# Optimization experiments

Measured on AMD Instinct MI355X. Metric: run time of the kernel, lower is better.

The kernel has to match this reference:

```python
import jax, jax.numpy as jnp
import numpy as np

N_NODES = 100000
N_EDGES = 1600000
DIMS = [21, 32, 64, 128, 21]  # conv1..conv4 (conv4 in-dim fixed to 128; source's 100 is a bug)


def _glorot(key, fan_in, fan_out):
    s = jnp.sqrt(6.0 / (fan_in + fan_out))
    return jax.random.uniform(key, (fan_in, fan_out), jnp.float32, -s, s)


def setup_inputs() -> dict:
    key = jax.random.key(0)
    ks = jax.random.split(key, 6)
    x = jax.random.normal(ks[0], (N_NODES, DIMS[0]), jnp.float32)
    edge_index = jax.random.randint(ks[1], (2, N_EDGES), 0, N_NODES, jnp.int64)
    inp = {"x": x, "edge_index": edge_index}
    wkeys = jax.random.split(ks[2], 4)
    for i in range(4):
        inp[f"W{i+1}"] = _glorot(wkeys[i], DIMS[i], DIMS[i + 1])
        inp[f"b{i+1}"] = jnp.zeros((DIMS[i + 1],), jnp.float32)
    return inp


def gcn_conv(x, row, col, W, b):
    # PyG GCNConv: h = x W; symmetric normalization with self loops; aggregate; + bias
    N = x.shape[0]
    h = x @ W  # [N, F]
    deg = jnp.zeros((N,), h.dtype).at[col].add(1.0) + 1.0  # +1 for self loop
    dinv = jax.lax.rsqrt(deg)
    norm = dinv[row] * dinv[col]  # [E]
    agg = jnp.zeros_like(h).at[col].add(norm[:, None] * h[row])  # scatter messages
    agg = agg + (dinv * dinv)[:, None] * h  # self-loop contribution
    return agg + b


def reference(x, edge_index, W1, b1, W2, b2, W3, b3, W4, b4):
    row, col = edge_index[0], edge_index[1]
    x = jax.nn.relu(gcn_conv(x, row, col, W1, b1))
    x = jax.nn.relu(gcn_conv(x, row, col, W2, b2))
    x = jax.nn.relu(gcn_conv(x, row, col, W3, b3))
    x = gcn_conv(x, row, col, W4, b4)
    return x
```

## Files before the change

kernel.cpp:

```cpp
#include <hip/hip_runtime.h>
#include <hip/hip_fp16.h>

#define NN 100000
#define NE 1600000
#define SH 7
#define NB_BKT 782
#define BCAP 3072
#define CSRCAP 3200
#define CHUNK 8192
#define TILES_TOTAL 3125
#define PIPE_BLOCKS 512

static inline int cdiv(long long a, int b) { return (int)((a + b - 1) / b); }

__device__ inline float4 ld_h4(const float2* __restrict__ base, size_t idx) {
    float2 v = base[idx];
    const __half2* p = (const __half2*)&v;
    float2 f0 = __half22float2(p[0]);
    float2 f1 = __half22float2(p[1]);
    return make_float4(f0.x, f0.y, f1.x, f1.y);
}

__global__ void partition_kernel(const int* __restrict__ row, const int* __restrict__ col,
                                 int* __restrict__ bcur,
                                 unsigned int* __restrict__ packed, int E) {
    __shared__ int lh[NB_BKT];
    __shared__ int lbase[NB_BKT];
    for (int i = threadIdx.x; i < NB_BKT; i += 256) lh[i] = 0;
    __syncthreads();
    int base = blockIdx.x * CHUNK;
    int end = min(base + CHUNK, E);
    for (int e = base + threadIdx.x; e < end; e += 256) atomicAdd(&lh[col[e] >> SH], 1);
    __syncthreads();
    for (int i = threadIdx.x; i < NB_BKT; i += 256) {
        int v = lh[i];
        lbase[i] = v ? atomicAdd(&bcur[i], v) : 0;
        lh[i] = 0;
    }
    __syncthreads();
    for (int e = base + threadIdx.x; e < end; e += 256) {
        int c = col[e];
        int r = row[e];
        int b = c >> SH;
        int off = atomicAdd(&lh[b], 1);
        packed[lbase[b] + off] = ((unsigned)r << 7) | (unsigned)(c & 127);
    }
}

__global__ void bucket_nodes_place(const unsigned int* __restrict__ packed,
                                   const int* __restrict__ bcur, int* __restrict__ rowptr,
                                   int* __restrict__ rowend, float* __restrict__ dinv,
                                   int* __restrict__ csr_row, int N) {
    int b = blockIdx.x;
    __shared__ int lcnt[128];
    __shared__ int lcur[128];
    __shared__ int wt4[4];
    int t = threadIdx.x;
    if (t < 128) lcnt[t] = 0;
    __syncthreads();
    int s = b * BCAP;
    int e = bcur[b];
    for (int i = s + t; i < e; i += 256)
        atomicAdd(&lcnt[packed[i] & 127u], 1);
    __syncthreads();
    int node = (b << SH) + t;
    int v = (t < 128 && node < N) ? lcnt[t] + 1 : 0;
    int lane = t & 63, w = t >> 6;
    int incl = v;
#pragma unroll
    for (int off = 1; off < 64; off <<= 1) {
        int u = __shfl_up(incl, off, 64);
        if (lane >= off) incl += u;
    }
    if (lane == 63) wt4[w] = incl;
    __syncthreads();
    int woff = 0;
    for (int i = 0; i < w; i++) woff += wt4[i];
    int excl = woff + incl - v;
    if (t < 128 && node < N) {
        int start = b * CSRCAP + excl;
        rowptr[node] = start;
        rowend[node] = start + v;
        csr_row[start] = node;
        dinv[node] = rsqrtf((float)v);
        lcur[t] = start + 1;
    }
    __syncthreads();
    for (int i = s + t; i < e; i += 256) {
        unsigned p = packed[i];
        int r = (int)(p >> 7);
        int pos = atomicAdd(&lcur[p & 127u], 1);
        csr_row[pos] = r;
    }
}

__global__ void padx_kernel(const float* __restrict__ x, float* __restrict__ xp,
                            int* __restrict__ bcur, int N) {
    int idx = blockIdx.x * blockDim.x + threadIdx.x;
    if (idx < NB_BKT) bcur[idx] = idx * BCAP;
    if (idx >= N * 32) return;
    int n = idx >> 5;
    int k = idx & 31;
    xp[idx] = (k < 21) ? x[n * 21 + k] : 0.f;
}

template <int LPN, int FIN, int FOUT, int RJ, int OSTRIDE, bool HALF_OUT, bool HALF_IN>
__global__ __launch_bounds__(512) void gather_gemm(
    const float4* __restrict__ h, const int* __restrict__ rowptr,
    const int* __restrict__ rowend, const int* __restrict__ csr_row,
    const float* __restrict__ dinv, const float* __restrict__ W,
    const float* __restrict__ b, float* __restrict__ out, int N) {
    constexpr int NT = 512 / LPN;
    constexpr int FINP = 4 * LPN;
    constexpr int XLD = FINP + 1;
    constexpr int JG = FOUT / RJ;
    __shared__ float xs[NT * XLD];
    __shared__ float Ws[FIN * FOUT];
    __shared__ float bs[FOUT];
    const int t = threadIdx.x;
    const float2* hf2 = (const float2*)h;

    for (int i = t; i < FIN * FOUT; i += 512) Ws[i] = W[i];
    if (t < FOUT) bs[t] = b[t];

    const int l = t % LPN;
    const int ny = t / LPN;
    const int node = blockIdx.x * NT + ny;
    float4 acc = make_float4(0.f, 0.f, 0.f, 0.f);
    if (node < N) {
        int s = rowptr[node], e = rowend[node];
        float dn = dinv[node];
        int i = s;
        for (; i + 3 < e; i += 4) {
            int r0 = csr_row[i], r1 = csr_row[i + 1], r2 = csr_row[i + 2], r3 = csr_row[i + 3];
            float w0 = dinv[r0] * dn, w1 = dinv[r1] * dn, w2 = dinv[r2] * dn, w3 = dinv[r3] * dn;
            float4 a0, a1, a2, a3;
            if constexpr (HALF_IN) {
                a0 = ld_h4(hf2, (size_t)r0 * LPN + l);
                a1 = ld_h4(hf2, (size_t)r1 * LPN + l);
                a2 = ld_h4(hf2, (size_t)r2 * LPN + l);
                a3 = ld_h4(hf2, (size_t)r3 * LPN + l);
            } else {
                a0 = h[(size_t)r0 * LPN + l];
                a1 = h[(size_t)r1 * LPN + l];
                a2 = h[(size_t)r2 * LPN + l];
                a3 = h[(size_t)r3 * LPN + l];
            }
            acc.x = fmaf(w0, a0.x, acc.x); acc.y = fmaf(w0, a0.y, acc.y);
            acc.z = fmaf(w0, a0.z, acc.z); acc.w = fmaf(w0, a0.w, acc.w);
            acc.x = fmaf(w1, a1.x, acc.x); acc.y = fmaf(w1, a1.y, acc.y);
            acc.z = fmaf(w1, a1.z, acc.z); acc.w = fmaf(w1, a1.w, acc.w);
            acc.x = fmaf(w2, a2.x, acc.x); acc.y = fmaf(w2, a2.y, acc.y);
            acc.z = fmaf(w2, a2.z, acc.z); acc.w = fmaf(w2, a2.w, acc.w);
            acc.x = fmaf(w3, a3.x, acc.x); acc.y = fmaf(w3, a3.y, acc.y);
            acc.z = fmaf(w3, a3.z, acc.z); acc.w = fmaf(w3, a3.w, acc.w);
        }
        for (; i < e; i++) {
            int r0 = csr_row[i];
            float w0 = dinv[r0] * dn;
            float4 a0;
            if constexpr (HALF_IN) a0 = ld_h4(hf2, (size_t)r0 * LPN + l);
            else                   a0 = h[(size_t)r0 * LPN + l];
            acc.x = fmaf(w0, a0.x, acc.x); acc.y = fmaf(w0, a0.y, acc.y);
            acc.z = fmaf(w0, a0.z, acc.z); acc.w = fmaf(w0, a0.w, acc.w);
        }
    }
    xs[ny * XLD + 4 * l + 0] = acc.x;
    xs[ny * XLD + 4 * l + 1] = acc.y;
    xs[ny * XLD + 4 * l + 2] = acc.z;
    xs[ny * XLD + 4 * l + 3] = acc.w;
    __syncthreads();

    const int jg = t % JG;
    const int ng = t / JG;
    float r[RJ];
#pragma unroll
    for (int jj = 0; jj < RJ; jj++) r[jj] = 0.f;
#pragma unroll 4
    for (int k = 0; k < FIN; k++) {
        float xv = xs[ng * XLD + k];
#pragma unroll
        for (int jj = 0; jj < RJ; jj++)
            r[jj] = fmaf(xv, Ws[k * FOUT + jg * RJ + jj], r[jj]);
    }
    int onode = blockIdx.x * NT + ng;
    if (onode < N) {
#pragma unroll
        for (int jj = 0; jj < RJ; jj++) r[jj] = fmaxf(r[jj] + bs[jg * RJ + jj], 0.f);
        if constexpr (HALF_OUT) {
            if constexpr (RJ == 8) {
                float4 pk;
                __half2* ph = (__half2*)&pk;
                ph[0] = __float22half2_rn(make_float2(r[0], r[1]));
                ph[1] = __float22half2_rn(make_float2(r[2], r[3]));
                ph[2] = __float22half2_rn(make_float2(r[4], r[5]));
                ph[3] = __float22half2_rn(make_float2(r[6], r[7]));
                *(float4*)((__half*)out + (size_t)onode * FOUT + jg * RJ) = pk;
            } else {
                static_assert(!HALF_OUT || RJ == 8 || RJ == 4, "half path needs RJ 4 or 8");
                float2 pk;
                __half2* ph = (__half2*)&pk;
                ph[0] = __float22half2_rn(make_float2(r[0], r[1]));
                ph[1] = __float22half2_rn(make_float2(r[2], r[3]));
                *(float2*)((__half*)out + (size_t)onode * FOUT + jg * RJ) = pk;
            }
        } else {
            float* orow = out + (size_t)onode * OSTRIDE + jg * RJ;
#pragma unroll
            for (int c = 0; c < RJ / 4; c++)
                *(float4*)&orow[4 * c] = make_float4(r[4 * c], r[4 * c + 1], r[4 * c + 2], r[4 * c + 3]);
        }
    }
}

template <int LPN, bool BIAS, bool STORE21, bool HALF_IN>
__global__ void gather4_kernel(const float4* __restrict__ h, const int* __restrict__ rowptr,
                               const int* __restrict__ rowend, const int* __restrict__ csr_row,
                               const float* __restrict__ dinv, const float* __restrict__ bias,
                               float* __restrict__ outp, int N) {
    int node = blockIdx.x * blockDim.y + threadIdx.y;
    if (node >= N) return;
    int l = threadIdx.x;
    int s = rowptr[node], e = rowend[node];
    float dn = dinv[node];
    const float2* hf2 = (const float2*)h;
    float4 acc = make_float4(0.f, 0.f, 0.f, 0.f);
    int i = s;
    for (; i + 3 < e; i += 4) {
        int r0 = csr_row[i], r1 = csr_row[i + 1], r2 = csr_row[i + 2], r3 = csr_row[i + 3];
        float w0 = dinv[r0] * dn, w1 = dinv[r1] * dn, w2 = dinv[r2] * dn, w3 = dinv[r3] * dn;
        float4 a0, a1, a2, a3;
        if constexpr (HALF_IN) {
            a0 = ld_h4(hf2, (size_t)r0 * LPN + l);
            a1 = ld_h4(hf2, (size_t)r1 * LPN + l);
            a2 = ld_h4(hf2, (size_t)r2 * LPN + l);
            a3 = ld_h4(hf2, (size_t)r3 * LPN + l);
        } else {
            a0 = h[(size_t)r0 * LPN + l];
            a1 = h[(size_t)r1 * LPN + l];
            a2 = h[(size_t)r2 * LPN + l];
            a3 = h[(size_t)r3 * LPN + l];
        }
        acc.x = fmaf(w0, a0.x, acc.x); acc.y = fmaf(w0, a0.y, acc.y);
        acc.z = fmaf(w0, a0.z, acc.z); acc.w = fmaf(w0, a0.w, acc.w);
        acc.x = fmaf(w1, a1.x, acc.x); acc.y = fmaf(w1, a1.y, acc.y);
        acc.z = fmaf(w1, a1.z, acc.z); acc.w = fmaf(w1, a1.w, acc.w);
        acc.x = fmaf(w2, a2.x, acc.x); acc.y = fmaf(w2, a2.y, acc.y);
        acc.z = fmaf(w2, a2.z, acc.z); acc.w = fmaf(w2, a2.w, acc.w);
        acc.x = fmaf(w3, a3.x, acc.x); acc.y = fmaf(w3, a3.y, acc.y);
        acc.z = fmaf(w3, a3.z, acc.z); acc.w = fmaf(w3, a3.w, acc.w);
    }
    for (; i < e; i++) {
        int r0 = csr_row[i];
        float w0 = dinv[r0] * dn;
        float4 a0;
        if constexpr (HALF_IN) a0 = ld_h4(hf2, (size_t)r0 * LPN + l);
        else                   a0 = h[(size_t)r0 * LPN + l];
        acc.x = fmaf(w0, a0.x, acc.x); acc.y = fmaf(w0, a0.y, acc.y);
        acc.z = fmaf(w0, a0.z, acc.z); acc.w = fmaf(w0, a0.w, acc.w);
    }
    if (STORE21) {
        int j = 4 * l;
        float v[4] = {acc.x, acc.y, acc.z, acc.w};
#pragma unroll
        for (int c = 0; c < 4; c++) {
            int jj = j + c;
            if (jj < 21) outp[(size_t)node * 21 + jj] = v[c] + (BIAS ? bias[jj] : 0.f);
        }
    } else {
        ((float4*)outp)[(size_t)node * LPN + l] = acc;
    }
}

__device__ inline void fma_h8(const float4& v, float w, float4& a0, float4& a1) {
    const __half2* hh = (const __half2*)&v;
    float2 f0 = __half22float2(hh[0]);
    float2 f1 = __half22float2(hh[1]);
    float2 f2 = __half22float2(hh[2]);
    float2 f3 = __half22float2(hh[3]);
    a0.x = fmaf(w, f0.x, a0.x); a0.y = fmaf(w, f0.y, a0.y);
    a0.z = fmaf(w, f1.x, a0.z); a0.w = fmaf(w, f1.y, a0.w);
    a1.x = fmaf(w, f2.x, a1.x); a1.y = fmaf(w, f2.y, a1.y);
    a1.z = fmaf(w, f3.x, a1.z); a1.w = fmaf(w, f3.y, a1.w);
}

__global__ __launch_bounds__(512, 4) void gather_gemm_l3l4_pipe(
    const float4* __restrict__ h, const int* __restrict__ rowptr,
    const int* __restrict__ rowend, const int* __restrict__ csr_row,
    const float* __restrict__ dinv, const float* __restrict__ W3,
    const float* __restrict__ b3, const float* __restrict__ W4,
    float* __restrict__ out, int N) {
    __shared__ float xs[2][32 * 65];
    __shared__ float4 W3v[64 * 32];
    __shared__ float4 W4v[16 * 48];
    __shared__ float b3s[128];
    const int t = threadIdx.x;
    const int b = blockIdx.x;

    for (int sid = t; sid < 64 * 32; sid += 512) {
        int k = sid >> 5, q = sid & 31;
        int jg = q >> 2, c = q & 3;
        W3v[(k << 5) + (c << 3) + jg] = ((const float4*)W3)[sid];
    }
    for (int cid = t; cid < 16 * 48; cid += 512) {
        int i = cid / 48, rem = cid - i * 48;
        int jq = rem >> 3, jg = rem & 7;
        int k = jg * 16 + i;
        float v0 = (4 * jq + 0 < 21) ? W4[k * 21 + 4 * jq + 0] : 0.f;
        float v1 = (4 * jq + 1 < 21) ? W4[k * 21 + 4 * jq + 1] : 0.f;
        float v2 = (4 * jq + 2 < 21) ? W4[k * 21 + 4 * jq + 2] : 0.f;
        float v3 = (4 * jq + 3 < 21) ? W4[k * 21 + 4 * jq + 3] : 0.f;
        W4v[cid] = make_float4(v0, v1, v2, v3);
    }
    if (t < 128) b3s[t] = b3[t];
    __syncthreads();

    const int R = (TILES_TOTAL - b + PIPE_BLOCKS - 1) / PIPE_BLOCKS;

    for (int r = 0; r <= R; r++) {
        if (t < 256) {
            if (r < R) {
                const int l = t & 7;
                const int ny = t >> 3;
                const int node = (b + PIPE_BLOCKS * r) * 32 + ny;
                float4 acc0 = make_float4(0.f, 0.f, 0.f, 0.f);
                float4 acc1 = make_float4(0.f, 0.f, 0.f, 0.f);
                if (node < N) {
                    int s = rowptr[node], e = rowend[node];
                    float dn = dinv[node];
                    int i = s;
                    for (; i + 5 < e; i += 6) {
                        int r0 = csr_row[i],     r1 = csr_row[i + 1], r2 = csr_row[i + 2];
                        int r3 = csr_row[i + 3], r4 = csr_row[i + 4], r5 = csr_row[i + 5];
                        float w0 = dinv[r0] * dn, w1 = dinv[r1] * dn, w2 = dinv[r2] * dn;
                        float w3 = dinv[r3] * dn, w4 = dinv[r4] * dn, w5 = dinv[r5] * dn;
                        float4 v0 = h[(size_t)r0 * 8 + l];
                        float4 v1 = h[(size_t)r1 * 8 + l];
                        float4 v2 = h[(size_t)r2 * 8 + l];
                        float4 v3 = h[(size_t)r3 * 8 + l];
                        float4 v4 = h[(size_t)r4 * 8 + l];
                        float4 v5 = h[(size_t)r5 * 8 + l];
                        fma_h8(v0, w0, acc0, acc1);
                        fma_h8(v1, w1, acc0, acc1);
                        fma_h8(v2, w2, acc0, acc1);
                        fma_h8(v3, w3, acc0, acc1);
                        fma_h8(v4, w4, acc0, acc1);
                        fma_h8(v5, w5, acc0, acc1);
                    }
                    for (; i < e; i++) {
                        int r0 = csr_row[i];
                        float w0 = dinv[r0] * dn;
                        float4 v0 = h[(size_t)r0 * 8 + l];
                        fma_h8(v0, w0, acc0, acc1);
                    }
                }
                float* xr = xs[r & 1] + ny * 65 + 8 * l;
                xr[0] = acc0.x; xr[1] = acc0.y; xr[2] = acc0.z; xr[3] = acc0.w;
                xr[4] = acc1.x; xr[5] = acc1.y; xr[6] = acc1.z; xr[7] = acc1.w;
            }
        } else {
            if (r >= 1) {
                const int jg = t & 7;
                const int ng = (t >> 3) & 31;
                const int node = (b + PIPE_BLOCKS * (r - 1)) * 32 + ng;
                const float* arow = xs[(r - 1) & 1] + ng * 65;

                float accA[16];
#pragma unroll
                for (int jj = 0; jj < 16; jj++) accA[jj] = 0.f;
#pragma unroll 4
                for (int k = 0; k < 64; k++) {
                    float xa = arow[k];
                    const float4* wb = &W3v[(k << 5) + jg];
#pragma unroll
                    for (int c = 0; c < 4; c++) {
                        float4 w = wb[c << 3];
                        accA[4 * c + 0] = fmaf(xa, w.x, accA[4 * c + 0]);
                        accA[4 * c + 1] = fmaf(xa, w.y, accA[4 * c + 1]);
                        accA[4 * c + 2] = fmaf(xa, w.z, accA[4 * c + 2]);
                        accA[4 * c + 3] = fmaf(xa, w.w, accA[4 * c + 3]);
                    }
                }
#pragma unroll
                for (int jj = 0; jj < 16; jj++) {
                    float bb = b3s[jg * 16 + jj];
                    accA[jj] = fmaxf(accA[jj] + bb, 0.f);
                }

                float pA[24];
#pragma unroll
                for (int j = 0; j < 24; j++) pA[j] = 0.f;
#pragma unroll
                for (int i = 0; i < 16; i++) {
                    float ha = accA[i];
                    const float4* wb = &W4v[i * 48 + jg];
#pragma unroll
                    for (int jq = 0; jq < 6; jq++) {
                        float4 w = wb[jq << 3];
                        pA[4 * jq + 0] = fmaf(ha, w.x, pA[4 * jq + 0]);
                        pA[4 * jq + 1] = fmaf(ha, w.y, pA[4 * jq + 1]);
                        pA[4 * jq + 2] = fmaf(ha, w.z, pA[4 * jq + 2]);
                        pA[4 * jq + 3] = fmaf(ha, w.w, pA[4 * jq + 3]);
                    }
                }
#pragma unroll
                for (int m = 1; m < 8; m <<= 1) {
#pragma unroll
                    for (int j = 0; j < 24; j++)
                        pA[j] += __shfl_xor(pA[j], m, 8);
                }
                if (node < N) {
                    __half* orow = (__half*)out + (size_t)node * 32;
                    float2 pk = make_float2(0.f, 0.f);
                    if (jg < 6) {
                        __half2* ph = (__half2*)&pk;
                        ph[0] = __float22half2_rn(make_float2(pA[4 * jg + 0], pA[4 * jg + 1]));
                        ph[1] = __float22half2_rn(make_float2(pA[4 * jg + 2], pA[4 * jg + 3]));
                    }
                    *(float2*)(orow + 4 * jg) = pk;
                }
            }
        }
        __syncthreads();
    }
}

extern "C" void kernel_launch(void* const* d_in, const int* in_sizes, int n_in,
                              void* d_out, int out_size, void* d_ws, size_t ws_size,
                              hipStream_t stream) {
    const float* x  = (const float*)d_in[0];
    const int*   ei = (const int*)d_in[1];
    const float* W1 = (const float*)d_in[2]; const float* b1 = (const float*)d_in[3];
    const float* W2 = (const float*)d_in[4]; const float* b2 = (const float*)d_in[5];
    const float* W3 = (const float*)d_in[6]; const float* b3 = (const float*)d_in[7];
    const float* W4 = (const float*)d_in[8]; const float* b4 = (const float*)d_in[9];
    const int* row = ei;
    const int* col = ei + NE;
    float* out = (float*)d_out;

    float* A      = (float*)d_ws;
    float* B      = A + (size_t)NN * 128;
    float* dinv   = B + (size_t)NN * 128;
    int*   rowptr = (int*)(dinv + NN);
    int*   rowend = rowptr + NN;
    int*   csr_row= rowend + NN;
    int*   bcur   = csr_row + (size_t)NB_BKT * CSRCAP;
    unsigned int* packed = (unsigned int*)A;

    const int BS = 256;
    const int NCH = cdiv(NE, CHUNK);

    padx_kernel<<<cdiv((long long)NN * 32, BS), BS, 0, stream>>>(x, B, bcur, NN);
    partition_kernel<<<NCH, 256, 0, stream>>>(row, col, bcur, packed, NE);
    bucket_nodes_place<<<NB_BKT, 256, 0, stream>>>(packed, bcur, rowptr, rowend, dinv, csr_row, NN);

    gather_gemm<8, 21, 32, 4, 32, true, false><<<cdiv(NN, 64), 512, 0, stream>>>(
        (const float4*)B, rowptr, rowend, csr_row, dinv, W1, b1, A, NN);
    gather_gemm<8, 32, 64, 8, 64, true, true><<<cdiv(NN, 64), 512, 0, stream>>>(
        (const float4*)A, rowptr, rowend, csr_row, dinv, W2, b2, B, NN);
    gather_gemm_l3l4_pipe<<<PIPE_BLOCKS, 512, 0, stream>>>(
        (const float4*)B, rowptr, rowend, csr_row, dinv, W3, b3, W4, A, NN);
    {
        dim3 blk(8, 32);
        gather4_kernel<8, true, true, true><<<cdiv(NN, 32), blk, 0, stream>>>(
            (const float4*)A, rowptr, rowend, csr_row, dinv, b4, out, NN);
    }
}
```

Baseline: 296.0 us.

## Apply W1 before aggregation and gather fp16 projected features in layer one

```diff
diff --git a/kernel.cpp b/kernel.cpp
--- a/kernel.cpp
+++ b/kernel.cpp
@@ -94,14 +94,37 @@
     }
 }
 
-__global__ void padx_kernel(const float* __restrict__ x, float* __restrict__ xp,
-                            int* __restrict__ bcur, int N) {
-    int idx = blockIdx.x * blockDim.x + threadIdx.x;
-    if (idx < NB_BKT) bcur[idx] = idx * BCAP;
-    if (idx >= N * 32) return;
-    int n = idx >> 5;
-    int k = idx & 31;
-    xp[idx] = (k < 21) ? x[n * 21 + k] : 0.f;
+__global__ void xw1_kernel(const float* __restrict__ x, const float* __restrict__ W1,
+                           __half* __restrict__ y, int* __restrict__ bcur, int N) {
+    __shared__ float xsm[64 * 21];
+    __shared__ float Wsm[21 * 32];
+    const int t = threadIdx.x;
+    const int n0 = blockIdx.x * 64;
+    if (blockIdx.x == 0)
+        for (int i = t; i < NB_BKT; i += 256) bcur[i] = i * BCAP;
+    for (int i = t; i < 21 * 32; i += 256) Wsm[i] = W1[i];
+    const int nv = min(64, N - n0);
+    for (int i = t; i < nv * 21; i += 256) xsm[i] = x[(size_t)n0 * 21 + i];
+    __syncthreads();
+    const int ng = t >> 2, jq = t & 3;
+    const int node = n0 + ng;
+    if (node >= N) return;
+    float r[8];
+#pragma unroll
+    for (int j = 0; j < 8; j++) r[j] = 0.f;
+    for (int k = 0; k < 21; k++) {
+        float xv = xsm[ng * 21 + k];
+#pragma unroll
+        for (int j = 0; j < 8; j++)
+            r[j] = fmaf(xv, Wsm[k * 32 + jq * 8 + j], r[j]);
+    }
+    float4 pk;
+    __half2* ph = (__half2*)&pk;
+    ph[0] = __float22half2_rn(make_float2(r[0], r[1]));
+    ph[1] = __float22half2_rn(make_float2(r[2], r[3]));
+    ph[2] = __float22half2_rn(make_float2(r[4], r[5]));
+    ph[3] = __float22half2_rn(make_float2(r[6], r[7]));
+    *(float4*)(y + (size_t)node * 32 + jq * 8) = pk;
 }
 
 template <int LPN, int FIN, int FOUT, int RJ, int OSTRIDE, bool HALF_OUT, bool HALF_IN>
@@ -213,7 +236,7 @@
     }
 }
 
-template <int LPN, bool BIAS, bool STORE21, bool HALF_IN>
+template <int LPN, bool BIAS, bool STORE21, bool HALF_IN, bool HRELU_OUT>
 __global__ void gather4_kernel(const float4* __restrict__ h, const int* __restrict__ rowptr,
                                const int* __restrict__ rowend, const int* __restrict__ csr_row,
                                const float* __restrict__ dinv, const float* __restrict__ bias,
@@ -259,7 +282,18 @@
         acc.x = fmaf(w0, a0.x, acc.x); acc.y = fmaf(w0, a0.y, acc.y);
         acc.z = fmaf(w0, a0.z, acc.z); acc.w = fmaf(w0, a0.w, acc.w);
     }
-    if (STORE21) {
+    if constexpr (HRELU_OUT) {
+        int j = 4 * l;
+        float v0 = fmaxf(acc.x + bias[j + 0], 0.f);
+        float v1 = fmaxf(acc.y + bias[j + 1], 0.f);
+        float v2 = fmaxf(acc.z + bias[j + 2], 0.f);
+        float v3 = fmaxf(acc.w + bias[j + 3], 0.f);
+        float2 pk;
+        __half2* ph = (__half2*)&pk;
+        ph[0] = __float22half2_rn(make_float2(v0, v1));
+        ph[1] = __float22half2_rn(make_float2(v2, v3));
+        *(float2*)((__half*)outp + (size_t)node * (4 * LPN) + j) = pk;
+    } else if (STORE21) {
         int j = 4 * l;
         float v[4] = {acc.x, acc.y, acc.z, acc.w};
 #pragma unroll
@@ -447,22 +481,24 @@
     int*   bcur   = csr_row + (size_t)NB_BKT * CSRCAP;
     unsigned int* packed = (unsigned int*)A;
 
-    const int BS = 256;
     const int NCH = cdiv(NE, CHUNK);
 
-    padx_kernel<<<cdiv((long long)NN * 32, BS), BS, 0, stream>>>(x, B, bcur, NN);
+    xw1_kernel<<<cdiv(NN, 64), 256, 0, stream>>>(x, W1, (__half*)B, bcur, NN);
     partition_kernel<<<NCH, 256, 0, stream>>>(row, col, bcur, packed, NE);
     bucket_nodes_place<<<NB_BKT, 256, 0, stream>>>(packed, bcur, rowptr, rowend, dinv, csr_row, NN);
 
-    gather_gemm<8, 21, 32, 4, 32, true, false><<<cdiv(NN, 64), 512, 0, stream>>>(
-        (const float4*)B, rowptr, rowend, csr_row, dinv, W1, b1, A, NN);
+    {
+        dim3 blk(8, 32);
+        gather4_kernel<8, true, false, true, true><<<cdiv(NN, 32), blk, 0, stream>>>(
+            (const float4*)B, rowptr, rowend, csr_row, dinv, b1, A, NN);
+    }
     gather_gemm<8, 32, 64, 8, 64, true, true><<<cdiv(NN, 64), 512, 0, stream>>>(
         (const float4*)A, rowptr, rowend, csr_row, dinv, W2, b2, B, NN);
     gather_gemm_l3l4_pipe<<<PIPE_BLOCKS, 512, 0, stream>>>(
         (const float4*)B, rowptr, rowend, csr_row, dinv, W3, b3, W4, A, NN);
     {
         dim3 blk(8, 32);
-        gather4_kernel<8, true, true, true><<<cdiv(NN, 32), blk, 0, stream>>>(
+        gather4_kernel<8, true, true, true, false><<<cdiv(NN, 32), blk, 0, stream>>>(
             (const float4*)A, rowptr, rowend, csr_row, dinv, b4, out, NN);
     }
 }
```

After: 289.9 us. 2.0% less time.
